# Kernel optimization log

Hardware: AMD Instinct MI355X
Metric: run time of the kernel (lower is better)

The kernel has to match this reference:

```python
import jax, jax.numpy as jnp
import numpy as np
import math


def _local_band_mask(L):
    # window_size = ceil(1.2 * log2(L) / 2); True where attention is DISALLOWED
    w = math.ceil(1.2 * np.log2(L) / 2)
    i = jnp.arange(L)[:, None]
    j = jnp.arange(L)[None, :]
    return jnp.abs(i - j) > w  # [L, L] bool, True outside the band


def setup_inputs() -> dict:
    key = jax.random.key(0)
    kq, kk, kv = jax.random.split(key, 3)
    B, L, H, E = 2, 2048, 8, 64
    return {
        "queries": jax.random.normal(kq, (B, L, H, E), dtype=jnp.float32),
        "keys": jax.random.normal(kk, (B, L, H, E), dtype=jnp.float32),
        "values": jax.random.normal(kv, (B, L, H, E), dtype=jnp.float32),
    }


def reference(queries, keys, values):
    # queries/keys: [B, L, H, E], values: [B, L, H, D]
    B, L, H, E = queries.shape
    scale = 1.0 / math.sqrt(E)
    # scores: [B, H, L, L]
    scores = jnp.einsum("bqhe,bkhe->bhqk", queries, keys) * scale
    mask = _local_band_mask(L)  # [L, L]
    scores = jnp.where(mask[None, None, :, :], -jnp.inf, scores)
    attn = jax.nn.softmax(scores, axis=-1)  # dropout is identity in eval
    # output: [B, L, H, D]
    out = jnp.einsum("bhqk,bkhd->bqhd", attn, values)
    return out
```

## Files before the change

kernel.cpp:

```cpp
#include <hip/hip_runtime.h>
#include <math.h>


constexpr int L_DIM = 2048;
constexpr int H_DIM = 8;
constexpr int E_DIM = 64;
constexpr int W = 7;
constexpr int QPW = 8;
constexpr int NU = 2 * W + QPW;
constexpr int TQ = 64;
constexpr int HALO = 8;
constexpr int ROWS = TQ + 2 * HALO;
constexpr int NCHUNK = ROWS * E_DIM * 4 / 1024;

__global__ __launch_bounds__(512, 4) void local_attn_kernel(
    const float* __restrict__ q,
    const float* __restrict__ k,
    const float* __restrict__ v,
    float* __restrict__ out) {
  __shared__ float smem[2 * ROWS * E_DIM];
  float* ks = smem;
  float* vs = smem + ROWS * E_DIM;

  const int cpx = gridDim.x >> 3;
  const int bid = (blockIdx.x & 7) * cpx + (blockIdx.x >> 3);

  const int tile = bid & (L_DIM / TQ - 1);
  const int bh = bid >> 5;
  const int h = bh & (H_DIM - 1);
  const int b = bh >> 3;
  const int l0 = tile * TQ;

  const int tid = threadIdx.x;
  const int wv = tid >> 6;
  const int lane = tid & 63;
  const int qsub = lane >> 3;
  const int c = lane & 7;

  const size_t bhb = (size_t)b * L_DIM * H_DIM + h;

  const int l0w = l0 + wv * QPW;
  const int l = l0w + qsub;

  const float* qp = q + ((bhb + (size_t)l * H_DIM) << 6) + c * 8;
  float4 q0 = *(const float4*)qp;
  float4 q1 = *(const float4*)(qp + 4);

  const int rsub = lane >> 4;
  const int col = (lane & 15) * 4;
  for (int ch = wv; ch < 2 * NCHUNK; ch += 8) {
    const int m = (ch >= NCHUNK) ? 1 : 0;
    const int cc = ch - m * NCHUNK;
    int rg = l0 - HALO + cc * 4 + rsub;
    rg = rg < 0 ? 0 : (rg > L_DIM - 1 ? L_DIM - 1 : rg);
    const float* src = (m ? v : k) + ((bhb + (size_t)rg * H_DIM) << 6) + col;
    float* dst = (m ? vs : ks) + cc * 256;
    __builtin_amdgcn_global_load_lds(
        (const __attribute__((address_space(1))) void*)src,
        (__attribute__((address_space(3))) void*)dst, 16, 0, 0);
  }
  __syncthreads();

  const float scale = 0.125f;
  q0.x *= scale; q0.y *= scale; q0.z *= scale; q0.w *= scale;
  q1.x *= scale; q1.y *= scale; q1.z *= scale; q1.w *= scale;

  float sc[NU];
#pragma unroll
  for (int i = 0; i < NU; ++i) {
    const int rl = wv * QPW + 1 + i;
    const float4 k0 = *(const float4*)&ks[rl * E_DIM + c * 8];
    const float4 k1 = *(const float4*)&ks[rl * E_DIM + c * 8 + 4];
    float s = q0.x * k0.x + q0.y * k0.y + q0.z * k0.z + q0.w * k0.w +
              q1.x * k1.x + q1.y * k1.y + q1.z * k1.z + q1.w * k1.w;
    s += __shfl_xor(s, 4);
    s += __shfl_xor(s, 2);
    s += __shfl_xor(s, 1);
    const int kk = l0w - W + i;
    const bool valid =
        (i >= qsub) && (i <= qsub + 2 * W) && (kk >= 0) && (kk < L_DIM);
    sc[i] = valid ? s : -INFINITY;
  }

  float mx = sc[0];
#pragma unroll
  for (int i = 1; i < NU; ++i) mx = fmaxf(mx, sc[i]);
  float den = 0.0f;
#pragma unroll
  for (int i = 0; i < NU; ++i) {
    sc[i] = __expf(sc[i] - mx);
    den += sc[i];
  }
  const float inv = 1.0f / den;

  float4 a0 = {0.f, 0.f, 0.f, 0.f};
  float4 a1 = {0.f, 0.f, 0.f, 0.f};
#pragma unroll
  for (int i = 0; i < NU; ++i) {
    const int rl = wv * QPW + 1 + i;
    const float4 v0 = *(const float4*)&vs[rl * E_DIM + c * 8];
    const float4 v1 = *(const float4*)&vs[rl * E_DIM + c * 8 + 4];
    const float p = sc[i];
    a0.x += p * v0.x; a0.y += p * v0.y; a0.z += p * v0.z; a0.w += p * v0.w;
    a1.x += p * v1.x; a1.y += p * v1.y; a1.z += p * v1.z; a1.w += p * v1.w;
  }

  float* op = out + ((bhb + (size_t)l * H_DIM) << 6) + c * 8;
  a0.x *= inv; a0.y *= inv; a0.z *= inv; a0.w *= inv;
  a1.x *= inv; a1.y *= inv; a1.z *= inv; a1.w *= inv;
  *(float4*)op = a0;
  *(float4*)(op + 4) = a1;
}

extern "C" void kernel_launch(void* const* d_in, const int* in_sizes, int n_in,
                              void* d_out, int out_size, void* d_ws, size_t ws_size,
                              hipStream_t stream) {
  const float* q = (const float*)d_in[0];
  const float* k = (const float*)d_in[1];
  const float* v = (const float*)d_in[2];
  float* out = (float*)d_out;

  const int B = in_sizes[0] / (L_DIM * H_DIM * E_DIM);
  const int blocks = B * H_DIM * (L_DIM / TQ);

  local_attn_kernel<<<blocks, 512, 0, stream>>>(q, k, v, out);
}
```

Baseline: 14.52 us.

## Stage K/V through registers into XOR-swizzled LDS, per-query window loop, DPP reductions

Result: faster. 12.27 us (-15.5%).

```diff
diff --git a/kernel.cpp b/kernel.cpp
--- a/kernel.cpp
+++ b/kernel.cpp
@@ -6,21 +6,24 @@
 constexpr int H_DIM = 8;
 constexpr int E_DIM = 64;
 constexpr int W = 7;
-constexpr int QPW = 8;
-constexpr int NU = 2 * W + QPW;
+constexpr int NK = 2 * W + 1;
 constexpr int TQ = 64;
 constexpr int HALO = 8;
 constexpr int ROWS = TQ + 2 * HALO;
-constexpr int NCHUNK = ROWS * E_DIM * 4 / 1024;
+
+template <int CTRL>
+__device__ __forceinline__ float dpp_add(float s) {
+  int t = __builtin_amdgcn_mov_dpp(__builtin_bit_cast(int, s), CTRL, 0xF, 0xF, true);
+  return s + __builtin_bit_cast(float, t);
+}
 
 __global__ __launch_bounds__(512, 4) void local_attn_kernel(
     const float* __restrict__ q,
     const float* __restrict__ k,
     const float* __restrict__ v,
     float* __restrict__ out) {
-  __shared__ float smem[2 * ROWS * E_DIM];
-  float* ks = smem;
-  float* vs = smem + ROWS * E_DIM;
+  __shared__ float ks[ROWS * E_DIM];
+  __shared__ float vs[ROWS * E_DIM];
 
   const int cpx = gridDim.x >> 3;
   const int bid = (blockIdx.x & 7) * cpx + (blockIdx.x >> 3);
@@ -39,68 +42,78 @@
 
   const size_t bhb = (size_t)b * L_DIM * H_DIM + h;
 
-  const int l0w = l0 + wv * QPW;
+  const int rsub = lane >> 4;
+  const int c4 = lane & 15;
+  float4 stg[5];
+  int stg_slot[5];
+#pragma unroll
+  for (int t = 0; t < 5; ++t) {
+    const int ch = wv + t * 8;
+    const int m = (ch >= 20) ? 1 : 0;
+    const int cc = ch - m * 20;
+    const int rl = cc * 4 + rsub;
+    int rg = l0 - HALO + rl;
+    rg = rg < 0 ? 0 : (rg > L_DIM - 1 ? L_DIM - 1 : rg);
+    const float* src =
+        (m ? v : k) + ((bhb + (size_t)rg * H_DIM) << 6) + c4 * 4;
+    stg[t] = *(const float4*)src;
+    stg_slot[t] = rl * 16 + (c4 ^ (rl & 7));
+  }
+
+  const int l0w = l0 + wv * 8;
   const int l = l0w + qsub;
-
   const float* qp = q + ((bhb + (size_t)l * H_DIM) << 6) + c * 8;
   float4 q0 = *(const float4*)qp;
   float4 q1 = *(const float4*)(qp + 4);
-
-  const int rsub = lane >> 4;
-  const int col = (lane & 15) * 4;
-  for (int ch = wv; ch < 2 * NCHUNK; ch += 8) {
-    const int m = (ch >= NCHUNK) ? 1 : 0;
-    const int cc = ch - m * NCHUNK;
-    int rg = l0 - HALO + cc * 4 + rsub;
-    rg = rg < 0 ? 0 : (rg > L_DIM - 1 ? L_DIM - 1 : rg);
-    const float* src = (m ? v : k) + ((bhb + (size_t)rg * H_DIM) << 6) + col;
-    float* dst = (m ? vs : ks) + cc * 256;
-    __builtin_amdgcn_global_load_lds(
-        (const __attribute__((address_space(1))) void*)src,
-        (__attribute__((address_space(3))) void*)dst, 16, 0, 0);
-  }
-  __syncthreads();
-
   const float scale = 0.125f;
   q0.x *= scale; q0.y *= scale; q0.z *= scale; q0.w *= scale;
   q1.x *= scale; q1.y *= scale; q1.z *= scale; q1.w *= scale;
 
-  float sc[NU];
 #pragma unroll
-  for (int i = 0; i < NU; ++i) {
-    const int rl = wv * QPW + 1 + i;
-    const float4 k0 = *(const float4*)&ks[rl * E_DIM + c * 8];
-    const float4 k1 = *(const float4*)&ks[rl * E_DIM + c * 8 + 4];
+  for (int t = 0; t < 5; ++t) {
+    const int ch = wv + t * 8;
+    float* dst = ((ch >= 20) ? vs : ks) + stg_slot[t] * 4;
+    *(float4*)dst = stg[t];
+  }
+  __syncthreads();
+
+  const int base_rl = wv * 8 + 1 + qsub;
+  float sc[NK];
+#pragma unroll
+  for (int j = 0; j < NK; ++j) {
+    const int rl = base_rl + j;
+    const int s8 = rl & 7;
+    const float4 k0 = *(const float4*)&ks[(rl * 16 + ((2 * c) ^ s8)) * 4];
+    const float4 k1 = *(const float4*)&ks[(rl * 16 + ((2 * c + 1) ^ s8)) * 4];
     float s = q0.x * k0.x + q0.y * k0.y + q0.z * k0.z + q0.w * k0.w +
               q1.x * k1.x + q1.y * k1.y + q1.z * k1.z + q1.w * k1.w;
-    s += __shfl_xor(s, 4);
-    s += __shfl_xor(s, 2);
-    s += __shfl_xor(s, 1);
-    const int kk = l0w - W + i;
-    const bool valid =
-        (i >= qsub) && (i <= qsub + 2 * W) && (kk >= 0) && (kk < L_DIM);
-    sc[i] = valid ? s : -INFINITY;
+    s = dpp_add<0xB1>(s);
+    s = dpp_add<0x4E>(s);
+    s = dpp_add<0x141>(s);
+    const int kk = l0w + qsub - W + j;
+    sc[j] = ((unsigned)kk < (unsigned)L_DIM) ? s : -INFINITY;
   }
 
   float mx = sc[0];
 #pragma unroll
-  for (int i = 1; i < NU; ++i) mx = fmaxf(mx, sc[i]);
+  for (int j = 1; j < NK; ++j) mx = fmaxf(mx, sc[j]);
   float den = 0.0f;
 #pragma unroll
-  for (int i = 0; i < NU; ++i) {
-    sc[i] = __expf(sc[i] - mx);
-    den += sc[i];
+  for (int j = 0; j < NK; ++j) {
+    sc[j] = __expf(sc[j] - mx);
+    den += sc[j];
   }
-  const float inv = 1.0f / den;
+  const float inv = __builtin_amdgcn_rcpf(den);
 
   float4 a0 = {0.f, 0.f, 0.f, 0.f};
   float4 a1 = {0.f, 0.f, 0.f, 0.f};
 #pragma unroll
-  for (int i = 0; i < NU; ++i) {
-    const int rl = wv * QPW + 1 + i;
-    const float4 v0 = *(const float4*)&vs[rl * E_DIM + c * 8];
-    const float4 v1 = *(const float4*)&vs[rl * E_DIM + c * 8 + 4];
-    const float p = sc[i];
+  for (int j = 0; j < NK; ++j) {
+    const int rl = base_rl + j;
+    const int s8 = rl & 7;
+    const float4 v0 = *(const float4*)&vs[(rl * 16 + ((2 * c) ^ s8)) * 4];
+    const float4 v1 = *(const float4*)&vs[(rl * 16 + ((2 * c + 1) ^ s8)) * 4];
+    const float p = sc[j];
     a0.x += p * v0.x; a0.y += p * v0.y; a0.z += p * v0.z; a0.w += p * v0.w;
     a1.x += p * v1.x; a1.y += p * v1.y; a1.z += p * v1.z; a1.w += p * v1.w;
   }
```
